# Performance work log

Measured on AMD Instinct MI355X. Metric: run time of the kernel, lower is better.

Reference implementation:

```python
import jax, jax.numpy as jnp
import numpy as np

# Static cluster layout: B graphs, PER atoms each; first NIN are 'inside'
# (aux_ind==0), remaining NOUT are 'outside' periodic images (aux_ind==1).
B, PER, NIN, K = 256, 1024, 256, 32
NOUT = PER - NIN
N = B * PER
R = 6.0        # cutoff radius (Angstrom)
BOX = 32.0     # box side -> ~30 neighbors within R at this density


def setup_inputs() -> dict:
    key = jax.random.key(0)
    pos = jax.random.uniform(key, (N, 3), dtype=jnp.float32) * BOX
    batch = (jnp.arange(N, dtype=jnp.int32) // PER)
    aux_ind = ((jnp.arange(N, dtype=jnp.int32) % PER) >= NIN).astype(jnp.int32)
    return {"pos": pos, "batch": batch, "aux_ind": aux_ind}


def _select_neighbors(d, valid, k):
    """Pick up to k valid candidates per target, lowest candidate index first.
    d: [..., C] distances, valid: [..., C] bool. Returns (idx, mask, dist),
    each [..., k]; padded slots have mask=False and dist=0."""
    C = d.shape[-1]
    order_key = jnp.where(valid, jnp.arange(C, dtype=jnp.int32), C + 1)
    idx = jnp.argsort(order_key, axis=-1)[..., :k]          # [..., k]
    mask = jnp.take_along_axis(valid, idx, axis=-1)
    dist = jnp.where(mask, jnp.take_along_axis(d, idx, axis=-1), 0.0)
    return idx.astype(jnp.int32), mask, dist


def reference(pos, batch, aux_ind):
    # batch/aux_ind are encoded by the static contiguous layout above;
    # they parameterize the same structure torch builds via scatter_add/cumsum.
    pg = pos.reshape(B, PER, 3)
    ins = pg[:, :NIN]            # [B, NIN, 3]  inside (target + intra-conv) nodes
    outs = pg[:, NIN:]           # [B, NOUT, 3] outside (inter-conv) nodes

    # intra edges: inside -> inside, same graph, no self loops
    d_ii = jnp.sqrt(jnp.sum((ins[:, :, None, :] - ins[:, None, :, :]) ** 2, -1))  # [B,NIN,NIN]
    valid_ii = (d_ii < R) & ~jnp.eye(NIN, dtype=bool)
    idx_ii, m_ii, dist_ii = _select_neighbors(d_ii, valid_ii, K)

    # inter edges: outside -> inside, same graph
    d_io = jnp.sqrt(jnp.sum((ins[:, :, None, :] - outs[:, None, :, :]) ** 2, -1))  # [B,NIN,NOUT]
    valid_io = d_io < R
    idx_io, m_io, dist_io = _select_neighbors(d_io, valid_io, K)

    # relabel to global node indices (flow='source_to_target': row=source, col=target)
    goff = (jnp.arange(B, dtype=jnp.int32) * PER)[:, None, None]       # [B,1,1]
    tgt = jnp.broadcast_to(goff + jnp.arange(NIN, dtype=jnp.int32)[None, :, None],
                           (B, NIN, K))
    src_ii = goff + idx_ii
    src_io = goff + NIN + idx_io

    edge_index = jnp.stack([src_ii.reshape(-1), tgt.reshape(-1)], 0)        # [2, B*NIN*K]
    edge_index_inter = jnp.stack([src_io.reshape(-1), tgt.reshape(-1)], 0)  # [2, B*NIN*K]

    return (edge_index, m_ii.reshape(-1), dist_ii,
            edge_index_inter, m_io.reshape(-1), dist_io)
```

## Files before the change

### kernel.cpp

```cpp
#include <hip/hip_runtime.h>
#include <math.h>


constexpr int BB    = 256;
constexpr int PERN  = 1024;
constexpr int NINC  = 256;
constexpr int NOUTC = 768;
constexpr int KK    = 32;
constexpr long EE   = (long)BB * NINC * KK;

__device__ __forceinline__ int prefix_lt(unsigned long long m) {
    return __builtin_amdgcn_mbcnt_hi((unsigned)(m >> 32),
           __builtin_amdgcn_mbcnt_lo((unsigned)m, 0u));
}

__device__ __forceinline__ float fast_sqrt(float x) {
    return __builtin_amdgcn_sqrtf(x);
}

__global__ __launch_bounds__(1024) void mo3e_kernel(const float* __restrict__ pos,
                                                    float* __restrict__ out) {
#pragma clang fp contract(off)
    __shared__ float4 sp[PERN];

    const int b   = blockIdx.x >> 4;
    const int tid = threadIdx.x;
    const int l   = tid & 63;
    const int i = __builtin_amdgcn_readfirstlane((blockIdx.x & 15) * 16 + (tid >> 6));

    const float* gp = pos + (long)b * PERN * 3;
    sp[tid] = make_float4(gp[tid * 3 + 0], gp[tid * 3 + 1], gp[tid * 3 + 2], 0.0f);
    __syncthreads();

    const float4 p = sp[i];
    const float xi = p.x, yi = p.y, zi = p.z;

    const int  goff = b * PERN;
    const long e0   = ((long)(b * NINC + i)) * KK;

    float* __restrict__ p_src_ii = out + e0;
    float* __restrict__ p_tgt_ii = out + EE + e0;
    float* __restrict__ p_m_ii   = out + 2 * EE + e0;
    float* __restrict__ p_d_ii   = out + 3 * EE + e0;
    float* __restrict__ p_src_io = out + 4 * EE + e0;
    float* __restrict__ p_tgt_io = out + 5 * EE + e0;
    float* __restrict__ p_m_io   = out + 6 * EE + e0;
    float* __restrict__ p_d_io   = out + 7 * EE + e0;

    const float fl = (float)l;
    const float tv = (float)(goff + i);
    if (l < KK) {
        p_tgt_ii[l] = tv;
        p_tgt_io[l] = tv;
    }

    {
        unsigned long long masks[NINC / 64];
        int cnt = 0;
#pragma unroll
        for (int it = 0; it < NINC / 64; ++it) {
            const int j = it * 64 + l;
            const float4 q = sp[j];
            const float dx = xi - q.x, dy = yi - q.y, dz = zi - q.z;
            const float d2 = (dx * dx + dy * dy) + dz * dz;
            unsigned long long ms = __ballot(d2 < 36.0f);
            if (it == (i >> 6)) ms &= ~(1ull << (i & 63));
            masks[it] = ms;
            const int slot = cnt + prefix_lt(ms);
            const bool mine = (ms >> l) & 1ull;
            if (mine && slot < KK) {
                p_src_ii[slot] = (float)(goff + it * 64) + fl;
                p_d_ii[slot]   = fast_sqrt(d2);
            }
            cnt += __popcll(ms);
            if (cnt >= KK) break;
        }
        const int S0 = cnt < KK ? cnt : KK;
        if (l < KK) {
            p_m_ii[l] = (l < S0) ? 1.0f : 0.0f;
            if (l >= S0) p_d_ii[l] = 0.0f;
        }
        if (S0 < KK) {
            int pc = S0;
#pragma unroll
            for (int it = 0; it < NINC / 64; ++it) {
                const unsigned long long inv = ~masks[it];
                const int slot = pc + prefix_lt(inv);
                const bool mine = (inv >> l) & 1ull;
                if (mine && slot < KK) p_src_ii[slot] = (float)(goff + it * 64) + fl;
                pc += __popcll(inv);
                if (pc >= KK) break;
            }
        }
    }

    {
        unsigned long long masks[NOUTC / 64];
        int cnt = 0;
#pragma unroll
        for (int it = 0; it < NOUTC / 64; ++it) {
            const int c = NINC + it * 64 + l;
            const float4 q = sp[c];
            const float dx = xi - q.x, dy = yi - q.y, dz = zi - q.z;
            const float d2 = (dx * dx + dy * dy) + dz * dz;
            const unsigned long long ms = __ballot(d2 < 36.0f);
            masks[it] = ms;
            const int slot = cnt + prefix_lt(ms);
            const bool mine = (ms >> l) & 1ull;
            if (mine && slot < KK) {
                p_src_io[slot] = (float)(goff + NINC + it * 64) + fl;
                p_d_io[slot]   = fast_sqrt(d2);
            }
            cnt += __popcll(ms);
            if (cnt >= KK) break;
        }
        const int S0 = cnt < KK ? cnt : KK;
        if (l < KK) {
            p_m_io[l] = (l < S0) ? 1.0f : 0.0f;
            if (l >= S0) p_d_io[l] = 0.0f;
        }
        if (S0 < KK) {
            int pc = S0;
#pragma unroll
            for (int it = 0; it < NOUTC / 64; ++it) {
                const unsigned long long inv = ~masks[it];
                const int slot = pc + prefix_lt(inv);
                const bool mine = (inv >> l) & 1ull;
                if (mine && slot < KK) p_src_io[slot] = (float)(goff + NINC + it * 64) + fl;
                pc += __popcll(inv);
                if (pc >= KK) break;
            }
        }
    }
}

extern "C" void kernel_launch(void* const* d_in, const int* in_sizes, int n_in,
                              void* d_out, int out_size, void* d_ws, size_t ws_size,
                              hipStream_t stream) {
    const float* pos = (const float*)d_in[0];
    float* out = (float*)d_out;

    mo3e_kernel<<<dim3(BB * 16), dim3(1024), 0, stream>>>(pos, out);
}
```

Baseline: 110.4 us.

## Stage neighbor indices in LDS and emit all outputs with coalesced stores

Selected neighbor indices for the intra and inter searches now go into a per-wave shared-memory slot buffer instead of being scattered straight to global memory. A final pass has all 64 lanes each handle one output slot (32 intra, 32 inter), recompute the distance from the staged index and write source, target, mask and distance with contiguous full-wave stores. This is meant to replace many small predicated global writes with a few coalesced ones. The cost is extra LDS traffic and a recomputed distance per slot, and it relies on 32-bit offset arithmetic fitting the output size.

```diff
diff --git a/kernel.cpp b/kernel.cpp
--- a/kernel.cpp
+++ b/kernel.cpp
@@ -1,5 +1,4 @@
 #include <hip/hip_runtime.h>
-#include <math.h>
 
 
 constexpr int BB    = 256;
@@ -7,87 +6,94 @@
 constexpr int NINC  = 256;
 constexpr int NOUTC = 768;
 constexpr int KK    = 32;
-constexpr long EE   = (long)BB * NINC * KK;
+constexpr unsigned EE = 256u * 256u * 32u;
 
 __device__ __forceinline__ int prefix_lt(unsigned long long m) {
     return __builtin_amdgcn_mbcnt_hi((unsigned)(m >> 32),
            __builtin_amdgcn_mbcnt_lo((unsigned)m, 0u));
 }
 
-__device__ __forceinline__ float fast_sqrt(float x) {
-    return __builtin_amdgcn_sqrtf(x);
-}
-
 __global__ __launch_bounds__(1024) void mo3e_kernel(const float* __restrict__ pos,
                                                     float* __restrict__ out) {
 #pragma clang fp contract(off)
     __shared__ float4 sp[PERN];
+    __shared__ int    slotbuf[16][64];
 
     const int b   = blockIdx.x >> 4;
     const int tid = threadIdx.x;
+    const int w   = tid >> 6;
     const int l   = tid & 63;
-    const int i = __builtin_amdgcn_readfirstlane((blockIdx.x & 15) * 16 + (tid >> 6));
+    const int i   = __builtin_amdgcn_readfirstlane((blockIdx.x & 15) * 16 + w);
 
-    const float* gp = pos + (long)b * PERN * 3;
+    const float* gp = pos + (size_t)b * PERN * 3;
     sp[tid] = make_float4(gp[tid * 3 + 0], gp[tid * 3 + 1], gp[tid * 3 + 2], 0.0f);
     __syncthreads();
 
     const float4 p = sp[i];
     const float xi = p.x, yi = p.y, zi = p.z;
 
-    const int  goff = b * PERN;
-    const long e0   = ((long)(b * NINC + i)) * KK;
+    int* slots = slotbuf[w];
 
-    float* __restrict__ p_src_ii = out + e0;
-    float* __restrict__ p_tgt_ii = out + EE + e0;
-    float* __restrict__ p_m_ii   = out + 2 * EE + e0;
-    float* __restrict__ p_d_ii   = out + 3 * EE + e0;
-    float* __restrict__ p_src_io = out + 4 * EE + e0;
-    float* __restrict__ p_tgt_io = out + 5 * EE + e0;
-    float* __restrict__ p_m_io   = out + 6 * EE + e0;
-    float* __restrict__ p_d_io   = out + 7 * EE + e0;
-
-    const float fl = (float)l;
-    const float tv = (float)(goff + i);
-    if (l < KK) {
-        p_tgt_ii[l] = tv;
-        p_tgt_io[l] = tv;
-    }
-
+    int S0ii;
     {
-        unsigned long long masks[NINC / 64];
+        unsigned long long masks[4];
         int cnt = 0;
 #pragma unroll
-        for (int it = 0; it < NINC / 64; ++it) {
+        for (int it = 0; it < 4; ++it) {
             const int j = it * 64 + l;
             const float4 q = sp[j];
             const float dx = xi - q.x, dy = yi - q.y, dz = zi - q.z;
             const float d2 = (dx * dx + dy * dy) + dz * dz;
-            unsigned long long ms = __ballot(d2 < 36.0f);
-            if (it == (i >> 6)) ms &= ~(1ull << (i & 63));
+            const bool valid = (d2 < 36.0f) && (j != i);
+            const unsigned long long ms = __ballot(valid);
             masks[it] = ms;
             const int slot = cnt + prefix_lt(ms);
-            const bool mine = (ms >> l) & 1ull;
-            if (mine && slot < KK) {
-                p_src_ii[slot] = (float)(goff + it * 64) + fl;
-                p_d_ii[slot]   = fast_sqrt(d2);
-            }
+            if (valid && slot < KK) slots[slot] = j;
             cnt += __popcll(ms);
             if (cnt >= KK) break;
         }
-        const int S0 = cnt < KK ? cnt : KK;
-        if (l < KK) {
-            p_m_ii[l] = (l < S0) ? 1.0f : 0.0f;
-            if (l >= S0) p_d_ii[l] = 0.0f;
-        }
-        if (S0 < KK) {
-            int pc = S0;
+        S0ii = cnt < KK ? cnt : KK;
+        if (S0ii < KK) {
+            int pc = S0ii;
 #pragma unroll
-            for (int it = 0; it < NINC / 64; ++it) {
+            for (int it = 0; it < 4; ++it) {
                 const unsigned long long inv = ~masks[it];
                 const int slot = pc + prefix_lt(inv);
                 const bool mine = (inv >> l) & 1ull;
-                if (mine && slot < KK) p_src_ii[slot] = (float)(goff + it * 64) + fl;
+                if (mine && slot < KK) slots[slot] = it * 64 + l;
+                pc += __popcll(inv);
+                if (pc >= KK) break;
+            }
+        }
+    }
+
+    int S0io;
+    {
+        unsigned long long masks[12];
+        int cnt = 0;
+#pragma unroll
+        for (int it = 0; it < 12; ++it) {
+            const int c = NINC + it * 64 + l;
+            const float4 q = sp[c];
+            const float dx = xi - q.x, dy = yi - q.y, dz = zi - q.z;
+            const float d2 = (dx * dx + dy * dy) + dz * dz;
+            const bool valid = (d2 < 36.0f);
+            const unsigned long long ms = __ballot(valid);
+            masks[it] = ms;
+            const int slot = cnt + prefix_lt(ms);
+            if (valid && slot < KK) slots[KK + slot] = c;
+            cnt += __popcll(ms);
+            if (cnt >= KK) break;
+        }
+        S0io = cnt < KK ? cnt : KK;
+        if (S0io < KK) {
+            int pc = S0io;
+#pragma unroll
+            for (int it = 0; it < 12; ++it) {
+                const unsigned long long inv = ~masks[it];
+                const int slot = pc + prefix_lt(inv);
+                const bool mine = (inv >> l) & 1ull;
+                if (mine && slot < KK) slots[KK + slot] = NINC + it * 64 + l;
                 pc += __popcll(inv);
                 if (pc >= KK) break;
             }
@@ -95,42 +101,25 @@
     }
 
     {
-        unsigned long long masks[NOUTC / 64];
-        int cnt = 0;
-#pragma unroll
-        for (int it = 0; it < NOUTC / 64; ++it) {
-            const int c = NINC + it * 64 + l;
-            const float4 q = sp[c];
-            const float dx = xi - q.x, dy = yi - q.y, dz = zi - q.z;
-            const float d2 = (dx * dx + dy * dy) + dz * dz;
-            const unsigned long long ms = __ballot(d2 < 36.0f);
-            masks[it] = ms;
-            const int slot = cnt + prefix_lt(ms);
-            const bool mine = (ms >> l) & 1ull;
-            if (mine && slot < KK) {
-                p_src_io[slot] = (float)(goff + NINC + it * 64) + fl;
-                p_d_io[slot]   = fast_sqrt(d2);
-            }
-            cnt += __popcll(ms);
-            if (cnt >= KK) break;
-        }
-        const int S0 = cnt < KK ? cnt : KK;
-        if (l < KK) {
-            p_m_io[l] = (l < S0) ? 1.0f : 0.0f;
-            if (l >= S0) p_d_io[l] = 0.0f;
-        }
-        if (S0 < KK) {
-            int pc = S0;
-#pragma unroll
-            for (int it = 0; it < NOUTC / 64; ++it) {
-                const unsigned long long inv = ~masks[it];
-                const int slot = pc + prefix_lt(inv);
-                const bool mine = (inv >> l) & 1ull;
-                if (mine && slot < KK) p_src_io[slot] = (float)(goff + NINC + it * 64) + fl;
-                pc += __popcll(inv);
-                if (pc >= KK) break;
-            }
-        }
+        const int h = l >> 5;
+        const int k = l & 31;
+        const int idx = slots[l];
+        const float4 q = sp[idx];
+        const float dx = xi - q.x, dy = yi - q.y, dz = zi - q.z;
+        const float d2 = (dx * dx + dy * dy) + dz * dz;
+
+        const int S0 = h ? S0io : S0ii;
+        const bool mv = k < S0;
+        const float dist = mv ? __builtin_amdgcn_sqrtf(d2) : 0.0f;
+
+        const int goff = b * PERN;
+        const unsigned e0  = (unsigned)(b * NINC + i) * KK;
+        const unsigned off = (h ? 4u * EE : 0u) + e0 + (unsigned)k;
+
+        out[off]           = (float)(goff + idx);
+        out[off + EE]      = (float)(goff + i);
+        out[off + 2u * EE] = mv ? 1.0f : 0.0f;
+        out[off + 3u * EE] = dist;
     }
 }
 
```

After: 103.8 us. 6.0% less time.
